# Kernel optimization log

Hardware: AMD Instinct MI355X
Metric: run time of the kernel (lower is better)

Reference implementation:

```python
import jax, jax.numpy as jnp
import numpy as np

N_NODES = 50000
N_EDGES = 600000
DIM_H = 128
LN_EPS = 1e-5


def setup_inputs() -> dict:
    key = jax.random.key(0)
    ks = jax.random.split(key, 8)
    s = 1.0 / np.sqrt(DIM_H)
    return {
        "nodes": jax.random.normal(ks[0], (N_NODES, DIM_H), jnp.float32),
        "W_msg": jax.random.normal(ks[1], (DIM_H, DIM_H), jnp.float32) * s,
        "b_msg": jnp.zeros((DIM_H,), jnp.float32),
        "w_ih": jax.random.normal(ks[2], (3 * DIM_H, DIM_H), jnp.float32) * s,
        "w_hh": jax.random.normal(ks[3], (3 * DIM_H, DIM_H), jnp.float32) * s,
        "b_ih": jnp.zeros((3 * DIM_H,), jnp.float32),
        "b_hh": jnp.zeros((3 * DIM_H,), jnp.float32),
        "ln_gamma": jnp.ones((DIM_H,), jnp.float32),
        "ln_beta": jnp.zeros((DIM_H,), jnp.float32),
        "edge_src": jax.random.randint(ks[4], (N_EDGES,), 0, N_NODES, jnp.int32),
        "edge_dst": jax.random.randint(ks[5], (N_EDGES,), 0, N_NODES, jnp.int32),
    }


def _layer_norm(x, gamma, beta):
    mu = jnp.mean(x, axis=-1, keepdims=True)
    var = jnp.mean(jnp.square(x - mu), axis=-1, keepdims=True)
    return gamma * (x - mu) * jax.lax.rsqrt(var + LN_EPS) + beta


def reference(nodes, W_msg, b_msg, w_ih, w_hh, b_ih, b_hh, ln_gamma, ln_beta,
              edge_src, edge_dst):
    n_nodes = nodes.shape[0]
    # send_and_recv: per-edge message from source node, sum-reduce at dest
    msg_e = nodes[edge_src] @ W_msg.T + b_msg            # [E, H] (irregular gather)
    messages = jax.ops.segment_sum(msg_e, edge_dst, num_segments=n_nodes)  # [N, H]
    # global connection: add mean node feature
    msg = messages + jnp.mean(nodes, axis=0)
    # single-step GRU (torch gate layout: r, z, n)
    gi = msg @ w_ih.T + b_ih                             # [N, 3H]
    gh = nodes @ w_hh.T + b_hh                           # [N, 3H]
    i_r, i_z, i_n = jnp.split(gi, 3, axis=-1)
    h_r, h_z, h_n = jnp.split(gh, 3, axis=-1)
    r = jax.nn.sigmoid(i_r + h_r)
    z = jax.nn.sigmoid(i_z + h_z)
    n = jnp.tanh(i_n + r * h_n)
    h_next = (1.0 - z) * n + z * nodes
    # LayerNorm then post-GRU spatial residual with messages
    out = _layer_norm(h_next, ln_gamma, ln_beta)
    out = out + messages
    return out
```

## Files before the change

### kernel.cpp

```cpp
#include <hip/hip_runtime.h>
#include <hip/hip_bf16.h>

#define N_NODES 50000
#define N_EDGES 600000
#define DIM_H   128
#define NPAD    50048
#define NB_SCAN 196

typedef __attribute__((ext_vector_type(8))) short bf16x8;
typedef __attribute__((ext_vector_type(4))) float f32x4;
typedef __attribute__((ext_vector_type(4))) short short4v;

__device__ __forceinline__ float b2f(__hip_bfloat16 x) { return __bfloat162float(x); }
__device__ __forceinline__ short f2bs(float f) {
    __hip_bfloat16 h = __float2bfloat16(f);
    return *reinterpret_cast<short*>(&h);
}
__device__ __forceinline__ float bs2f(short s) {
    unsigned u = ((unsigned)(unsigned short)s) << 16;
    return __builtin_bit_cast(float, u);
}

__device__ __forceinline__ void dma16(const void* g, const void* lds_uniform) {
    __builtin_amdgcn_global_load_lds(
        (const __attribute__((address_space(1))) void*)g,
        (__attribute__((address_space(3))) void*)(unsigned)(unsigned long long)lds_uniform,
        16, 0, 0);
}

__global__ __launch_bounds__(256) void colsum_k(const float* __restrict__ nodes,
                                                float* __restrict__ colsum,
                                                short* __restrict__ nodesB) {
    __shared__ float red[8][128];
    const int tid = threadIdx.x;
    const int cg = tid & 31;
    const int rl = tid >> 5;
    float4 acc = {0.f, 0.f, 0.f, 0.f};
    for (int r = blockIdx.x * 8 + rl; r < N_NODES; r += gridDim.x * 8) {
        float4 v = *(const float4*)(nodes + (size_t)r * DIM_H + cg * 4);
        acc.x += v.x; acc.y += v.y; acc.z += v.z; acc.w += v.w;
        *(short4v*)(nodesB + (size_t)r * DIM_H + cg * 4) =
            (short4v){f2bs(v.x), f2bs(v.y), f2bs(v.z), f2bs(v.w)};
    }
    *(float4*)&red[rl][cg * 4] = acc;
    __syncthreads();
    if (tid < 128) {
        float s = 0.f;
#pragma unroll
        for (int i = 0; i < 8; ++i) s += red[i][tid];
        unsafeAtomicAdd(&colsum[tid], s);
    }
}

__global__ __launch_bounds__(256) void wcvt_k(const float* __restrict__ wmsg,
                                              const float* __restrict__ wih,
                                              const float* __restrict__ whh,
                                              short* __restrict__ wmsgB,
                                              short* __restrict__ wihB,
                                              short* __restrict__ whhB) {
    int i = blockIdx.x * 256 + threadIdx.x;
    if (i < 16384) wmsgB[i] = f2bs(wmsg[i]);
    if (i < 49152) { wihB[i] = f2bs(wih[i]); whhB[i] = f2bs(whh[i]); }
}

__global__ __launch_bounds__(256) void hist_k(const int* __restrict__ edst,
                                              int* __restrict__ cnt) {
    int e = blockIdx.x * 256 + threadIdx.x;
    if (e < N_EDGES) atomicAdd(&cnt[edst[e]], 1);
}

__global__ __launch_bounds__(256) void bsum_k(const int* __restrict__ cnt,
                                              int* __restrict__ bsum) {
    const int t = threadIdx.x;
    int i = blockIdx.x * 256 + t;
    int v = (i < N_NODES) ? cnt[i] : 0;
#pragma unroll
    for (int o = 32; o; o >>= 1) v += __shfl_xor(v, o, 64);
    __shared__ int w4[4];
    if ((t & 63) == 0) w4[t >> 6] = v;
    __syncthreads();
    if (t == 0) bsum[blockIdx.x] = w4[0] + w4[1] + w4[2] + w4[3];
}

__global__ __launch_bounds__(256) void scan2_k(const int* __restrict__ cnt,
                                               const int* __restrict__ bsum,
                                               int* __restrict__ rowptr,
                                               int* __restrict__ pos) {
    const int b = blockIdx.x, t = threadIdx.x;
    const int lane = t & 63, w = t >> 6;
    __shared__ int red[4];
    __shared__ int wsum[4];

    int ov = (t < b) ? bsum[t] : 0;
#pragma unroll
    for (int o = 32; o; o >>= 1) ov += __shfl_xor(ov, o, 64);
    if (lane == 0) red[w] = ov;
    __syncthreads();
    const int offset = red[0] + red[1] + red[2] + red[3];

    int i = b * 256 + t;
    int v = (i < N_NODES) ? cnt[i] : 0;
    int x = v;
#pragma unroll
    for (int o = 1; o < 64; o <<= 1) {
        int y = __shfl_up(x, o, 64);
        if (lane >= o) x += y;
    }
    if (lane == 63) wsum[w] = x;
    __syncthreads();
    int woff = 0;
#pragma unroll
    for (int j = 0; j < 4; ++j)
        if (j < w) woff += wsum[j];
    int excl = offset + woff + (x - v);
    if (i < N_NODES) { rowptr[i] = excl; pos[i] = excl; }
    if (i == N_NODES - 1) rowptr[N_NODES] = excl + v;
}

__global__ __launch_bounds__(256) void reorder_k(const int* __restrict__ esrc,
                                                 const int* __restrict__ edst,
                                                 int* __restrict__ pos,
                                                 int* __restrict__ ssrc) {
    int e = blockIdx.x * 256 + threadIdx.x;
    if (e < N_EDGES) {
        int p = atomicAdd(&pos[edst[e]], 1);
        ssrc[p] = esrc[e];
    }
}

__global__ __launch_bounds__(256) void aggregate_k(const short* __restrict__ nodesB,
                                                   const int* __restrict__ rowptr,
                                                   const int* __restrict__ ssrc,
                                                   short* __restrict__ aggB) {
    const int wid = threadIdx.x >> 6;
    const int lane = threadIdx.x & 63;
    const int n = blockIdx.x * 4 + wid;
    if (n >= N_NODES) return;
    const int s0 = rowptr[n], s1 = rowptr[n + 1];
    float2 acc = {0.f, 0.f};
    int e = s0;
    for (; e + 3 < s1; e += 4) {
        int sa = ssrc[e], sb = ssrc[e + 1], sc = ssrc[e + 2], sd = ssrc[e + 3];
        short2 va = ((const short2*)(nodesB + (size_t)sa * DIM_H))[lane];
        short2 vb = ((const short2*)(nodesB + (size_t)sb * DIM_H))[lane];
        short2 vc = ((const short2*)(nodesB + (size_t)sc * DIM_H))[lane];
        short2 vd = ((const short2*)(nodesB + (size_t)sd * DIM_H))[lane];
        acc.x += (bs2f(va.x) + bs2f(vb.x)) + (bs2f(vc.x) + bs2f(vd.x));
        acc.y += (bs2f(va.y) + bs2f(vb.y)) + (bs2f(vc.y) + bs2f(vd.y));
    }
    for (; e < s1; ++e) {
        int sa = ssrc[e];
        short2 va = ((const short2*)(nodesB + (size_t)sa * DIM_H))[lane];
        acc.x += bs2f(va.x);
        acc.y += bs2f(va.y);
    }
    short2 o; o.x = f2bs(acc.x); o.y = f2bs(acc.y);
    ((short2*)(aggB + (size_t)n * DIM_H))[lane] = o;
}

__device__ __forceinline__ void stage_tile(const short* __restrict__ src, int row0,
                                           short* lds, int w, int lane) {
#pragma unroll
    for (int it = 0; it < 8; ++it) {
        int c = w * 8 + it;
        int s = c * 64 + lane;
        int r = s >> 4, q = s & 15;
        int g = q ^ (r & 15);
        dma16(src + (((size_t)(row0 + r)) << 7) + (g << 3), lds + (size_t)c * 512);
    }
}

__global__ __launch_bounds__(256) void mgemm0_k(const short* __restrict__ aggB,
                                                const short* __restrict__ wmsgB,
                                                const float* __restrict__ bmsg,
                                                const int* __restrict__ degi,
                                                const float* __restrict__ colsum,
                                                short* __restrict__ msginB) {
    __shared__ short As[128 * 128];
    __shared__ short Ws[128 * 128];
    const int tid = threadIdx.x;
    const int lane = tid & 63, w = tid >> 6;
    const int m0 = blockIdx.x * 128;

    stage_tile(aggB, m0, As, w, lane);
    stage_tile(wmsgB, 0, Ws, w, lane);
    __syncthreads();

    const int r16 = lane & 15, half = lane >> 4;
    const int wm = (w >> 1) * 64, wn = (w & 1) * 64;
    f32x4 acc[4][4] = {};
#pragma unroll
    for (int kt = 0; kt < 4; ++kt) {
        const int sq = ((kt * 4 + half) ^ r16) << 3;
        bf16x8 af[4], bfr[4];
#pragma unroll
        for (int t = 0; t < 4; ++t) {
            af[t]  = *(const bf16x8*)&As[(wm + t * 16 + r16) * 128 + sq];
            bfr[t] = *(const bf16x8*)&Ws[(wn + t * 16 + r16) * 128 + sq];
        }
#pragma unroll
        for (int i = 0; i < 4; ++i)
#pragma unroll
            for (int j = 0; j < 4; ++j)
                acc[i][j] = __builtin_amdgcn_mfma_f32_16x16x32_bf16(
                    af[i], bfr[j], acc[i][j], 0, 0, 0);
    }

#pragma unroll
    for (int i = 0; i < 4; ++i)
#pragma unroll
        for (int r = 0; r < 4; ++r) {
            int m = m0 + wm + i * 16 + half * 4 + r;
            if (m < N_NODES) {
#pragma unroll
                for (int j = 0; j < 4; ++j) {
                    int n = wn + j * 16 + r16;
                    float c = acc[i][j][r] + (float)degi[m] * bmsg[n]
                            + colsum[n] * (1.0f / N_NODES);
                    msginB[(size_t)m * 128 + n] = f2bs(c);
                }
            }
        }
}

__global__ __launch_bounds__(256) void gigh_k(const short* __restrict__ msginB,
                                              const short* __restrict__ nodesB,
                                              const short* __restrict__ wihB,
                                              const short* __restrict__ whhB,
                                              const float* __restrict__ bih,
                                              const float* __restrict__ bhh,
                                              short* __restrict__ gi,
                                              short* __restrict__ gh) {
    __shared__ short As[128 * 128];
    __shared__ short Ws[128 * 128];
    const int tid = threadIdx.x;
    const int lane = tid & 63, w = tid >> 6;
    const int m0 = blockIdx.x * 128;
    const int y = blockIdx.y;
    const short* A; const short* W; const float* bias; short* out; int n0;
    if (y < 3) { A = msginB; W = wihB; bias = bih; out = gi; n0 = y * 128; }
    else       { A = nodesB; W = whhB; bias = bhh; out = gh; n0 = (y - 3) * 128; }

    stage_tile(A, m0, As, w, lane);
    stage_tile(W, n0, Ws, w, lane);
    __syncthreads();

    const int r16 = lane & 15, half = lane >> 4;
    const int wm = (w >> 1) * 64, wn = (w & 1) * 64;
    f32x4 acc[4][4] = {};
#pragma unroll
    for (int kt = 0; kt < 4; ++kt) {
        const int sq = ((kt * 4 + half) ^ r16) << 3;
        bf16x8 af[4], bfr[4];
#pragma unroll
        for (int t = 0; t < 4; ++t) {
            af[t]  = *(const bf16x8*)&As[(wm + t * 16 + r16) * 128 + sq];
            bfr[t] = *(const bf16x8*)&Ws[(wn + t * 16 + r16) * 128 + sq];
        }
#pragma unroll
        for (int i = 0; i < 4; ++i)
#pragma unroll
            for (int j = 0; j < 4; ++j)
                acc[i][j] = __builtin_amdgcn_mfma_f32_16x16x32_bf16(
                    af[i], bfr[j], acc[i][j], 0, 0, 0);
    }

#pragma unroll
    for (int i = 0; i < 4; ++i)
#pragma unroll
        for (int r = 0; r < 4; ++r) {
            int m = m0 + wm + i * 16 + half * 4 + r;
            if (m < N_NODES) {
#pragma unroll
                for (int j = 0; j < 4; ++j) {
                    int n = n0 + wn + j * 16 + r16;
                    out[(size_t)m * 384 + n] = f2bs(acc[i][j][r] + bias[n]);
                }
            }
        }
}

__global__ __launch_bounds__(256) void fuse_k(const float* __restrict__ nodes,
                                              const __hip_bfloat16* __restrict__ gi,
                                              const __hip_bfloat16* __restrict__ gh,
                                              const __hip_bfloat16* __restrict__ msginB,
                                              const float* __restrict__ colsum,
                                              const float* __restrict__ gamma,
                                              const float* __restrict__ beta,
                                              float* __restrict__ out) {
    const int wid = threadIdx.x >> 6;
    const int lane = threadIdx.x & 63;
    const int n = blockIdx.x * 4 + wid;
    if (n >= N_NODES) return;

    const __hip_bfloat16* gir = gi + (size_t)n * 384;
    const __hip_bfloat16* ghr = gh + (size_t)n * 384;

    float hn[2], resid[2];
    float s = 0.f;
#pragma unroll
    for (int t = 0; t < 2; ++t) {
        int c = lane + t * 64;
        float ir = b2f(gir[c]), iz = b2f(gir[128 + c]), inn = b2f(gir[256 + c]);
        float hr = b2f(ghr[c]), hz = b2f(ghr[128 + c]), hhn = b2f(ghr[256 + c]);
        float r = 1.f / (1.f + expf(-(ir + hr)));
        float z = 1.f / (1.f + expf(-(iz + hz)));
        float ng = tanhf(inn + r * hhn);
        float h = nodes[(size_t)n * DIM_H + c];
        hn[t] = (1.f - z) * ng + z * h;
        float mi = b2f(msginB[(size_t)n * DIM_H + c]);
        resid[t] = mi - colsum[c] * (1.0f / N_NODES);
        s += hn[t];
    }
#pragma unroll
    for (int o = 32; o; o >>= 1) s += __shfl_xor(s, o, 64);
    float mu = s * (1.0f / DIM_H);
    float v = 0.f;
#pragma unroll
    for (int t = 0; t < 2; ++t) {
        float d = hn[t] - mu;
        v += d * d;
    }
#pragma unroll
    for (int o = 32; o; o >>= 1) v += __shfl_xor(v, o, 64);
    float rstd = rsqrtf(v * (1.0f / DIM_H) + 1e-5f);
#pragma unroll
    for (int t = 0; t < 2; ++t) {
        int c = lane + t * 64;
        float y = gamma[c] * (hn[t] - mu) * rstd + beta[c];
        out[(size_t)n * DIM_H + c] = y + resid[t];
    }
}

extern "C" void kernel_launch(void* const* d_in, const int* in_sizes, int n_in,
                              void* d_out, int out_size, void* d_ws, size_t ws_size,
                              hipStream_t stream) {
    const float* nodes = (const float*)d_in[0];
    const float* Wmsg  = (const float*)d_in[1];
    const float* bmsg  = (const float*)d_in[2];
    const float* wih   = (const float*)d_in[3];
    const float* whh   = (const float*)d_in[4];
    const float* bih   = (const float*)d_in[5];
    const float* bhh   = (const float*)d_in[6];
    const float* gamma = (const float*)d_in[7];
    const float* beta  = (const float*)d_in[8];
    const int* esrc = (const int*)d_in[9];
    const int* edst = (const int*)d_in[10];
    float* out = (float*)d_out;

    char* ws = (char*)d_ws;
    short* gi_s   = (short*)ws;
    short* aggB   = (short*)ws;
    short* gh_s   = (short*)(ws + 38400000);
    int*   bsum   = (int*)(ws + 38400000);
    short* nodesB = (short*)(ws + 76800000);
    short* msginB = (short*)(ws + 89612288);
    short* wmsgB  = (short*)(ws + 102424576);
    short* wihB   = (short*)(ws + 102457344);
    short* whhB   = (short*)(ws + 102555648);
    float* colsum = (float*)(ws + 102653952);
    int*   cnt    = (int*)(ws + 102654464);
    int*   rowptr = (int*)(ws + 102854464);
    int*   pos    = (int*)(ws + 103054472);
    int*   ssrc   = (int*)(ws + 103254472);

    hipMemsetAsync(cnt, 0, N_NODES * sizeof(int), stream);
    hipMemsetAsync(colsum, 0, DIM_H * sizeof(float), stream);
    hipMemsetAsync(ws + (size_t)N_NODES * 256, 0, (NPAD - N_NODES) * 256, stream);
    hipMemsetAsync(ws + 76800000 + (size_t)N_NODES * 256, 0, (NPAD - N_NODES) * 256, stream);
    hipMemsetAsync(ws + 89612288 + (size_t)N_NODES * 256, 0, (NPAD - N_NODES) * 256, stream);

    colsum_k<<<512, 256, 0, stream>>>(nodes, colsum, nodesB);
    wcvt_k<<<192, 256, 0, stream>>>(Wmsg, wih, whh, wmsgB, wihB, whhB);

    const int EB = (N_EDGES + 255) / 256;
    hist_k<<<EB, 256, 0, stream>>>(edst, cnt);
    bsum_k<<<NB_SCAN, 256, 0, stream>>>(cnt, bsum);
    scan2_k<<<NB_SCAN, 256, 0, stream>>>(cnt, bsum, rowptr, pos);
    reorder_k<<<EB, 256, 0, stream>>>(esrc, edst, pos, ssrc);
    aggregate_k<<<(N_NODES + 3) / 4, 256, 0, stream>>>(nodesB, rowptr, ssrc, aggB);

    const int MB2 = (N_NODES + 127) / 128;
    mgemm0_k<<<dim3(MB2, 1), 256, 0, stream>>>(aggB, wmsgB, bmsg, cnt, colsum, msginB);
    gigh_k<<<dim3(MB2, 6), 256, 0, stream>>>(msginB, nodesB, wihB, whhB, bih, bhh,
                                             gi_s, gh_s);

    fuse_k<<<(N_NODES + 3) / 4, 256, 0, stream>>>(nodes,
                                                  (const __hip_bfloat16*)gi_s,
                                                  (const __hip_bfloat16*)gh_s,
                                                  (const __hip_bfloat16*)msginB,
                                                  colsum, gamma, beta, out);
}
```

Baseline: 281.1 us.

## Fuse GRU gate GEMMs with gate activation and LayerNorm epilogue

Replaces the separate gi/gh GEMM kernel and the elementwise GRU+LayerNorm kernel with one kernel per 128-row tile. That kernel computes the r, n and z gate GEMMs in sequence, restaging weight slices into LDS, and applies the activations in registers. LayerNorm runs on a tile buffer held in shared memory. This removes the large bf16 gi/gh intermediate writes and reads plus one launch. In exchange it uses 128KB of LDS with one block per CU, serialises the gate phases, and the h term in the update now comes from the bf16 copy of the nodes instead of fp32.

```diff
diff --git a/kernel.cpp b/kernel.cpp
--- a/kernel.cpp
+++ b/kernel.cpp
@@ -20,6 +20,7 @@
     unsigned u = ((unsigned)(unsigned short)s) << 16;
     return __builtin_bit_cast(float, u);
 }
+__device__ __forceinline__ float sigm(float x) { return 1.f / (1.f + expf(-x)); }
 
 __device__ __forceinline__ void dma16(const void* g, const void* lds_uniform) {
     __builtin_amdgcn_global_load_lds(
@@ -170,6 +171,33 @@
     }
 }
 
+__device__ __forceinline__ void wave_mm(const short* __restrict__ A,
+                                        const short* __restrict__ W,
+                                        f32x4 (&acc)[4][4],
+                                        int wm, int wn, int r16, int half) {
+#pragma unroll
+    for (int kt = 0; kt < 4; ++kt) {
+        const int sq = ((kt * 4 + half) ^ r16) << 3;
+        bf16x8 af[4], bfr[4];
+#pragma unroll
+        for (int t = 0; t < 4; ++t) {
+            af[t]  = *(const bf16x8*)&A[(wm + t * 16 + r16) * 128 + sq];
+            bfr[t] = *(const bf16x8*)&W[(wn + t * 16 + r16) * 128 + sq];
+        }
+#pragma unroll
+        for (int i = 0; i < 4; ++i)
+#pragma unroll
+            for (int j = 0; j < 4; ++j)
+                acc[i][j] = __builtin_amdgcn_mfma_f32_16x16x32_bf16(
+                    af[i], bfr[j], acc[i][j], 0, 0, 0);
+    }
+}
+
+__device__ __forceinline__ int swz(int row, int col) {
+    int g = (col >> 3) ^ (row & 15);
+    return row * 128 + (g << 3) + (col & 7);
+}
+
 __global__ __launch_bounds__(256) void mgemm0_k(const short* __restrict__ aggB,
                                                 const short* __restrict__ wmsgB,
                                                 const float* __restrict__ bmsg,
@@ -189,22 +217,7 @@
     const int r16 = lane & 15, half = lane >> 4;
     const int wm = (w >> 1) * 64, wn = (w & 1) * 64;
     f32x4 acc[4][4] = {};
-#pragma unroll
-    for (int kt = 0; kt < 4; ++kt) {
-        const int sq = ((kt * 4 + half) ^ r16) << 3;
-        bf16x8 af[4], bfr[4];
-#pragma unroll
-        for (int t = 0; t < 4; ++t) {
-            af[t]  = *(const bf16x8*)&As[(wm + t * 16 + r16) * 128 + sq];
-            bfr[t] = *(const bf16x8*)&Ws[(wn + t * 16 + r16) * 128 + sq];
-        }
-#pragma unroll
-        for (int i = 0; i < 4; ++i)
-#pragma unroll
-            for (int j = 0; j < 4; ++j)
-                acc[i][j] = __builtin_amdgcn_mfma_f32_16x16x32_bf16(
-                    af[i], bfr[j], acc[i][j], 0, 0, 0);
-    }
+    wave_mm(As, Ws, acc, wm, wn, r16, half);
 
 #pragma unroll
     for (int i = 0; i < 4; ++i)
@@ -223,112 +236,138 @@
         }
 }
 
-__global__ __launch_bounds__(256) void gigh_k(const short* __restrict__ msginB,
-                                              const short* __restrict__ nodesB,
-                                              const short* __restrict__ wihB,
-                                              const short* __restrict__ whhB,
-                                              const float* __restrict__ bih,
-                                              const float* __restrict__ bhh,
-                                              short* __restrict__ gi,
-                                              short* __restrict__ gh) {
-    __shared__ short As[128 * 128];
-    __shared__ short Ws[128 * 128];
+__global__ __launch_bounds__(256, 1) void grufuse_k(const short* __restrict__ msginB,
+                                                    const short* __restrict__ nodesB,
+                                                    const short* __restrict__ wihB,
+                                                    const short* __restrict__ whhB,
+                                                    const float* __restrict__ bih,
+                                                    const float* __restrict__ bhh,
+                                                    const float* __restrict__ colsum,
+                                                    const float* __restrict__ gamma,
+                                                    const float* __restrict__ beta,
+                                                    float* __restrict__ out) {
+    __shared__ short Am[128 * 128];
+    __shared__ short An[128 * 128];
+    __shared__ short Wbuf[2 * 128 * 128];
+    short* Wi = Wbuf;
+    short* Wh = Wbuf + 128 * 128;
+    float* hbuf = (float*)Wbuf;
+
     const int tid = threadIdx.x;
     const int lane = tid & 63, w = tid >> 6;
     const int m0 = blockIdx.x * 128;
-    const int y = blockIdx.y;
-    const short* A; const short* W; const float* bias; short* out; int n0;
-    if (y < 3) { A = msginB; W = wihB; bias = bih; out = gi; n0 = y * 128; }
-    else       { A = nodesB; W = whhB; bias = bhh; out = gh; n0 = (y - 3) * 128; }
-
-    stage_tile(A, m0, As, w, lane);
-    stage_tile(W, n0, Ws, w, lane);
-    __syncthreads();
-
     const int r16 = lane & 15, half = lane >> 4;
     const int wm = (w >> 1) * 64, wn = (w & 1) * 64;
-    f32x4 acc[4][4] = {};
-#pragma unroll
-    for (int kt = 0; kt < 4; ++kt) {
-        const int sq = ((kt * 4 + half) ^ r16) << 3;
-        bf16x8 af[4], bfr[4];
-#pragma unroll
-        for (int t = 0; t < 4; ++t) {
-            af[t]  = *(const bf16x8*)&As[(wm + t * 16 + r16) * 128 + sq];
-            bfr[t] = *(const bf16x8*)&Ws[(wn + t * 16 + r16) * 128 + sq];
+
+    stage_tile(msginB, m0, Am, w, lane);
+    stage_tile(nodesB, m0, An, w, lane);
+    stage_tile(wihB, 0, Wi, w, lane);
+    stage_tile(whhB, 0, Wh, w, lane);
+    __syncthreads();
+
+    f32x4 rA[4][4] = {};
+    wave_mm(Am, Wi, rA, wm, wn, r16, half);
+    wave_mm(An, Wh, rA, wm, wn, r16, half);
+    __syncthreads();
+    stage_tile(wihB, 256, Wi, w, lane);
+    stage_tile(whhB, 256, Wh, w, lane);
+    {
+        float bj[4];
+#pragma unroll
+        for (int j = 0; j < 4; ++j) {
+            int c = wn + j * 16 + r16;
+            bj[j] = bih[c] + bhh[c];
         }
 #pragma unroll
         for (int i = 0; i < 4; ++i)
 #pragma unroll
             for (int j = 0; j < 4; ++j)
-                acc[i][j] = __builtin_amdgcn_mfma_f32_16x16x32_bf16(
-                    af[i], bfr[j], acc[i][j], 0, 0, 0);
-    }
-
-#pragma unroll
-    for (int i = 0; i < 4; ++i)
-#pragma unroll
-        for (int r = 0; r < 4; ++r) {
-            int m = m0 + wm + i * 16 + half * 4 + r;
-            if (m < N_NODES) {
+#pragma unroll
+                for (int r = 0; r < 4; ++r)
+                    rA[i][j][r] = sigm(rA[i][j][r] + bj[j]);
+    }
+    __syncthreads();
+
+    f32x4 inA[4][4] = {};
+    wave_mm(Am, Wi, inA, wm, wn, r16, half);
+    f32x4 hnA[4][4] = {};
+    wave_mm(An, Wh, hnA, wm, wn, r16, half);
+    __syncthreads();
+    stage_tile(wihB, 128, Wi, w, lane);
+    stage_tile(whhB, 128, Wh, w, lane);
+    {
+        float bi[4], bh[4];
+#pragma unroll
+        for (int j = 0; j < 4; ++j) {
+            int c = wn + j * 16 + r16;
+            bi[j] = bih[256 + c];
+            bh[j] = bhh[256 + c];
+        }
+#pragma unroll
+        for (int i = 0; i < 4; ++i)
+#pragma unroll
+            for (int j = 0; j < 4; ++j)
+#pragma unroll
+                for (int r = 0; r < 4; ++r)
+                    inA[i][j][r] = tanhf(inA[i][j][r] + bi[j] +
+                                         rA[i][j][r] * (hnA[i][j][r] + bh[j]));
+    }
+    __syncthreads();
+
+    f32x4 zA[4][4] = {};
+    wave_mm(Am, Wi, zA, wm, wn, r16, half);
+    wave_mm(An, Wh, zA, wm, wn, r16, half);
+    __syncthreads();
+
+    {
+        float bj[4];
+#pragma unroll
+        for (int j = 0; j < 4; ++j) {
+            int c = wn + j * 16 + r16;
+            bj[j] = bih[128 + c] + bhh[128 + c];
+        }
+#pragma unroll
+        for (int i = 0; i < 4; ++i)
+#pragma unroll
+            for (int r = 0; r < 4; ++r) {
+                int row = wm + i * 16 + half * 4 + r;
 #pragma unroll
                 for (int j = 0; j < 4; ++j) {
-                    int n = n0 + wn + j * 16 + r16;
-                    out[(size_t)m * 384 + n] = f2bs(acc[i][j][r] + bias[n]);
+                    int col = wn + j * 16 + r16;
+                    float z = sigm(zA[i][j][r] + bj[j]);
+                    float h = bs2f(An[swz(row, col)]);
+                    hbuf[row * 128 + col] = (1.f - z) * inA[i][j][r] + z * h;
                 }
             }
-        }
-}
-
-__global__ __launch_bounds__(256) void fuse_k(const float* __restrict__ nodes,
-                                              const __hip_bfloat16* __restrict__ gi,
-                                              const __hip_bfloat16* __restrict__ gh,
-                                              const __hip_bfloat16* __restrict__ msginB,
-                                              const float* __restrict__ colsum,
-                                              const float* __restrict__ gamma,
-                                              const float* __restrict__ beta,
-                                              float* __restrict__ out) {
-    const int wid = threadIdx.x >> 6;
-    const int lane = threadIdx.x & 63;
-    const int n = blockIdx.x * 4 + wid;
-    if (n >= N_NODES) return;
-
-    const __hip_bfloat16* gir = gi + (size_t)n * 384;
-    const __hip_bfloat16* ghr = gh + (size_t)n * 384;
-
-    float hn[2], resid[2];
-    float s = 0.f;
-#pragma unroll
-    for (int t = 0; t < 2; ++t) {
-        int c = lane + t * 64;
-        float ir = b2f(gir[c]), iz = b2f(gir[128 + c]), inn = b2f(gir[256 + c]);
-        float hr = b2f(ghr[c]), hz = b2f(ghr[128 + c]), hhn = b2f(ghr[256 + c]);
-        float r = 1.f / (1.f + expf(-(ir + hr)));
-        float z = 1.f / (1.f + expf(-(iz + hz)));
-        float ng = tanhf(inn + r * hhn);
-        float h = nodes[(size_t)n * DIM_H + c];
-        hn[t] = (1.f - z) * ng + z * h;
-        float mi = b2f(msginB[(size_t)n * DIM_H + c]);
-        resid[t] = mi - colsum[c] * (1.0f / N_NODES);
-        s += hn[t];
-    }
-#pragma unroll
-    for (int o = 32; o; o >>= 1) s += __shfl_xor(s, o, 64);
-    float mu = s * (1.0f / DIM_H);
-    float v = 0.f;
-#pragma unroll
-    for (int t = 0; t < 2; ++t) {
-        float d = hn[t] - mu;
-        v += d * d;
-    }
-#pragma unroll
-    for (int o = 32; o; o >>= 1) v += __shfl_xor(v, o, 64);
-    float rstd = rsqrtf(v * (1.0f / DIM_H) + 1e-5f);
-#pragma unroll
-    for (int t = 0; t < 2; ++t) {
-        int c = lane + t * 64;
-        float y = gamma[c] * (hn[t] - mu) * rstd + beta[c];
-        out[(size_t)n * DIM_H + c] = y + resid[t];
+    }
+    __syncthreads();
+
+    {
+        float ga = gamma[lane], gb = gamma[lane + 64];
+        float ba = beta[lane],  bb = beta[lane + 64];
+        float ca = colsum[lane] * (1.0f / N_NODES);
+        float cb = colsum[lane + 64] * (1.0f / N_NODES);
+        for (int rr = 0; rr < 32; ++rr) {
+            int row = w * 32 + rr;
+            int gm = m0 + row;
+            float a = hbuf[row * 128 + lane];
+            float b = hbuf[row * 128 + 64 + lane];
+            float s = a + b, q = a * a + b * b;
+#pragma unroll
+            for (int o = 32; o; o >>= 1) {
+                s += __shfl_xor(s, o, 64);
+                q += __shfl_xor(q, o, 64);
+            }
+            float mu = s * (1.0f / 128.0f);
+            float var = q * (1.0f / 128.0f) - mu * mu;
+            float rstd = rsqrtf(var + 1e-5f);
+            if (gm < N_NODES) {
+                float ma = bs2f(Am[swz(row, lane)]) - ca;
+                float mb = bs2f(Am[swz(row, lane + 64)]) - cb;
+                out[(size_t)gm * 128 + lane]      = ga * (a - mu) * rstd + ba + ma;
+                out[(size_t)gm * 128 + 64 + lane] = gb * (b - mu) * rstd + bb + mb;
+            }
+        }
     }
 }
 
@@ -349,26 +388,25 @@
     float* out = (float*)d_out;
 
     char* ws = (char*)d_ws;
-    short* gi_s   = (short*)ws;
     short* aggB   = (short*)ws;
-    short* gh_s   = (short*)(ws + 38400000);
-    int*   bsum   = (int*)(ws + 38400000);
-    short* nodesB = (short*)(ws + 76800000);
-    short* msginB = (short*)(ws + 89612288);
-    short* wmsgB  = (short*)(ws + 102424576);
-    short* wihB   = (short*)(ws + 102457344);
-    short* whhB   = (short*)(ws + 102555648);
-    float* colsum = (float*)(ws + 102653952);
-    int*   cnt    = (int*)(ws + 102654464);
-    int*   rowptr = (int*)(ws + 102854464);
-    int*   pos    = (int*)(ws + 103054472);
-    int*   ssrc   = (int*)(ws + 103254472);
+    short* nodesB = (short*)(ws + 12812288);
+    short* msginB = (short*)(ws + 25624576);
+    short* wmsgB  = (short*)(ws + 38436864);
+    short* wihB   = (short*)(ws + 38469632);
+    short* whhB   = (short*)(ws + 38567936);
+    float* colsum = (float*)(ws + 38666240);
+    int*   cnt    = (int*)(ws + 38666752);
+    int*   rowptr = (int*)(ws + 38866752);
+    int*   pos    = (int*)(ws + 39066760);
+    int*   ssrc   = (int*)(ws + 39266760);
+    int*   bsum   = pos;
+    bsum          = (int*)(ws + 41666760);
 
     hipMemsetAsync(cnt, 0, N_NODES * sizeof(int), stream);
     hipMemsetAsync(colsum, 0, DIM_H * sizeof(float), stream);
     hipMemsetAsync(ws + (size_t)N_NODES * 256, 0, (NPAD - N_NODES) * 256, stream);
-    hipMemsetAsync(ws + 76800000 + (size_t)N_NODES * 256, 0, (NPAD - N_NODES) * 256, stream);
-    hipMemsetAsync(ws + 89612288 + (size_t)N_NODES * 256, 0, (NPAD - N_NODES) * 256, stream);
+    hipMemsetAsync(ws + 12812288 + (size_t)N_NODES * 256, 0, (NPAD - N_NODES) * 256, stream);
+    hipMemsetAsync(ws + 25624576 + (size_t)N_NODES * 256, 0, (NPAD - N_NODES) * 256, stream);
 
     colsum_k<<<512, 256, 0, stream>>>(nodes, colsum, nodesB);
     wcvt_k<<<192, 256, 0, stream>>>(Wmsg, wih, whh, wmsgB, wihB, whhB);
@@ -382,12 +420,6 @@
 
     const int MB2 = (N_NODES + 127) / 128;
     mgemm0_k<<<dim3(MB2, 1), 256, 0, stream>>>(aggB, wmsgB, bmsg, cnt, colsum, msginB);
-    gigh_k<<<dim3(MB2, 6), 256, 0, stream>>>(msginB, nodesB, wihB, whhB, bih, bhh,
-                                             gi_s, gh_s);
-
-    fuse_k<<<(N_NODES + 3) / 4, 256, 0, stream>>>(nodes,
-                                                  (const __hip_bfloat16*)gi_s,
-                                                  (const __hip_bfloat16*)gh_s,
-                                                  (const __hip_bfloat16*)msginB,
-                                                  colsum, gamma, beta, out);
-}
+    grufuse_k<<<MB2, 256, 0, stream>>>(msginB, nodesB, wihB, whhB, bih, bhh,
+                                       colsum, gamma, beta, out);
+}
```

New measurement: 297.1 us. +5.7%, slower.
